# Kernel optimization log

Hardware: AMD Instinct MI355X
Metric: run time of the kernel (lower is better)

## Reference

```python
import jax, jax.numpy as jnp
import numpy as np

N = 1024; D = 128; H = 128; FF = 2048; NHEAD = 4; VOCAB = 32000; EPS = 1e-5


def _ln(x, s, b):
    m = x.mean(-1, keepdims=True)
    v = ((x - m) ** 2).mean(-1, keepdims=True)
    return (x - m) / jnp.sqrt(v + EPS) * s + b


def _mha(x, qkv_w, qkv_b, ow, ob):
    n, d = x.shape
    hd = d // NHEAD
    qkv = x @ qkv_w.T + qkv_b  # (n, 3d)
    q, k, v = [t.reshape(n, NHEAD, hd).transpose(1, 0, 2) for t in jnp.split(qkv, 3, axis=-1)]
    scores = jnp.einsum('hqd,hkd->hqk', q, k) / np.float32(np.sqrt(hd))
    attn = jax.nn.softmax(scores, axis=-1)
    o = jnp.einsum('hqk,hkd->hqd', attn, v).transpose(1, 0, 2).reshape(n, d)
    return o @ ow.T + ob


def setup_inputs() -> dict:
    key = jax.random.key(0)
    ks = jax.random.split(key, 10)
    s = 0.02
    p = lambda k, shape: (jax.random.normal(k, shape, jnp.float32) * s)
    return {
        'inputs': jax.random.randint(ks[0], (N,), 0, VOCAB),
        'emb': p(ks[1], (VOCAB, D)),
        'qkv_w': p(ks[2], (2, 3 * D, D)), 'qkv_b': jnp.zeros((2, 3 * D), jnp.float32),
        'attn_out_w': p(ks[3], (2, D, D)), 'attn_out_b': jnp.zeros((2, D), jnp.float32),
        'ln1_s': jnp.ones((2, D), jnp.float32), 'ln1_b': jnp.zeros((2, D), jnp.float32),
        'ln2_s': jnp.ones((2, D), jnp.float32), 'ln2_b': jnp.zeros((2, D), jnp.float32),
        'ff1_w': p(ks[4], (2, FF, D)), 'ff1_b': jnp.zeros((2, FF), jnp.float32),
        'ff2_w': p(ks[5], (2, D, FF)), 'ff2_b': jnp.zeros((2, D), jnp.float32),
        'w1': p(ks[6], (H, 2 * D)), 'b1': jnp.zeros((H,), jnp.float32),
        'w2': p(ks[7], (1, H)), 'b2': jnp.zeros((1,), jnp.float32),
    }


def reference(inputs, emb, qkv_w, qkv_b, attn_out_w, attn_out_b, ln1_s, ln1_b,
              ln2_s, ln2_b, ff1_w, ff1_b, ff2_w, ff2_b, w1, b1, w2, b2):
    x = emb[inputs]  # (n, d)
    for l in range(2):  # post-norm TransformerEncoderLayer (torch default)
        x = _ln(x + _mha(x, qkv_w[l], qkv_b[l], attn_out_w[l], attn_out_b[l]), ln1_s[l], ln1_b[l])
        ff = jax.nn.relu(x @ ff1_w[l].T + ff1_b[l]) @ ff2_w[l].T + ff2_b[l]
        x = _ln(x + ff, ln2_s[l], ln2_b[l])
    # pair MLP: concat(e_i, e_j) @ W1.T == e_i @ W1_left.T + e_j @ W1_right.T
    a = x @ w1[:, :D].T  # (n, H)
    b = x @ w1[:, D:].T  # (n, H)
    h = jax.nn.relu(a[:, None, :] + b[None, :, :] + b1)  # (n, n, H)
    return (h @ w2.T + b2)[..., 0]  # (n, n)
```

## Files before the change

### kernel.cpp

```cpp
#include <hip/hip_runtime.h>
#include <math.h>

#define N_TOK 1024
#define D_MODEL 128
#define NHEAD 4
#define HD 32
#define FF_DIM 2048
#define H_PAIR 128
#define QK_SCALE 0.17677669529663687f

typedef __attribute__((ext_vector_type(8))) short bf16x8;
typedef __attribute__((ext_vector_type(4))) float f32x4;

__device__ __forceinline__ unsigned short f2bf(float f) {
    unsigned u = __float_as_uint(f);
    u = u + 0x7FFFu + ((u >> 16) & 1u);
    return (unsigned short)(u >> 16);
}

__global__ void cvt4_kernel(const float* __restrict__ s0, int n0, const float* __restrict__ s1, int n1,
                            const float* __restrict__ s2, int n2, const float* __restrict__ s3, int n3,
                            unsigned short* __restrict__ d0, unsigned short* __restrict__ d1,
                            unsigned short* __restrict__ d2, unsigned short* __restrict__ d3) {
    int i = blockIdx.x * 256 + threadIdx.x;
    if (i < n0) { d0[i] = f2bf(s0[i]); return; } i -= n0;
    if (i < n1) { d1[i] = f2bf(s1[i]); return; } i -= n1;
    if (i < n2) { d2[i] = f2bf(s2[i]); return; } i -= n2;
    if (i < n3) { d3[i] = f2bf(s3[i]); }
}

__global__ void w1split_kernel(const float* __restrict__ w1, unsigned short* __restrict__ w1L,
                               unsigned short* __restrict__ w1R) {
    int h = blockIdx.x, t = threadIdx.x;
    float v = w1[h * 256 + t];
    if (t < 128) w1L[h * 128 + t] = f2bf(v);
    else         w1R[h * 128 + (t - 128)] = f2bf(v);
}

__global__ void embed_kernel(const int* __restrict__ ids, const float* __restrict__ emb,
                             float* __restrict__ x, unsigned short* __restrict__ xb) {
    int u = blockIdx.x * 256 + threadIdx.x;
    int i = u >> 5, d4 = (u & 31) * 4;
    float4 v = *(const float4*)&emb[(size_t)ids[i] * D_MODEL + d4];
    *(float4*)&x[i * D_MODEL + d4] = v;
    ushort4 bv;
    bv.x = f2bf(v.x); bv.y = f2bf(v.y); bv.z = f2bf(v.z); bv.w = f2bf(v.w);
    *(ushort4*)&xb[i * D_MODEL + d4] = bv;
}

__global__ __launch_bounds__(256) void gemm_bf(const unsigned short* __restrict__ Xb,
                                               const unsigned short* __restrict__ Wb,
                                               const unsigned short* __restrict__ Wb2,
                                               const float* __restrict__ bias,
                                               const float* __restrict__ res,
                                               float* __restrict__ Cf,
                                               unsigned short* __restrict__ Cb,
                                               float* __restrict__ part,
                                               int M, int Nc, int K, int kChunk, int act) {
    const int lane = threadIdx.x & 63;
    const int w = threadIdx.x >> 6;
    const int m0 = blockIdx.y * 64 + w * 16;
    const int n0 = blockIdx.x * 64;
    const int kb = part ? blockIdx.z * kChunk : 0;
    const int r16 = lane & 15, kh = lane >> 4;

    const unsigned short* Wsel = (Wb2 && blockIdx.z == 1) ? Wb2 : Wb;

    f32x4 acc[4] = {{0.f,0.f,0.f,0.f},{0.f,0.f,0.f,0.f},{0.f,0.f,0.f,0.f},{0.f,0.f,0.f,0.f}};
    const unsigned short* Ap = Xb + (size_t)(m0 + r16) * K + kb + kh * 8;
    const unsigned short* Bp = Wsel + (size_t)(n0 + r16) * K + kb + kh * 8;

    for (int k0 = 0; k0 < kChunk; k0 += 32) {
        bf16x8 a = *(const bf16x8*)(Ap + k0);
#pragma unroll
        for (int nt = 0; nt < 4; ++nt) {
            bf16x8 b = *(const bf16x8*)(Bp + (size_t)nt * 16 * K + k0);
            acc[nt] = __builtin_amdgcn_mfma_f32_16x16x32_bf16(a, b, acc[nt], 0, 0, 0);
        }
    }

    if (part) {
        float* P = part + (size_t)blockIdx.z * M * Nc;
#pragma unroll
        for (int nt = 0; nt < 4; ++nt) {
            int col = n0 + nt * 16 + r16;
#pragma unroll
            for (int r = 0; r < 4; ++r) {
                int row = m0 + kh * 4 + r;
                P[(size_t)row * Nc + col] = acc[nt][r];
            }
        }
    } else {
        size_t zoff = (size_t)blockIdx.z * M * Nc;
#pragma unroll
        for (int nt = 0; nt < 4; ++nt) {
            int col = n0 + nt * 16 + r16;
            float bv = bias ? bias[col] : 0.f;
#pragma unroll
            for (int r = 0; r < 4; ++r) {
                int row = m0 + kh * 4 + r;
                float v = acc[nt][r] + bv;
                if (res) v += res[(size_t)row * Nc + col];
                if (act) v = fmaxf(v, 0.f);
                if (Cf) Cf[zoff + (size_t)row * Nc + col] = v;
                if (Cb) Cb[zoff + (size_t)row * Nc + col] = f2bf(v);
            }
        }
    }
}

__global__ __launch_bounds__(256) void attn_flash(const float* __restrict__ qkv,
                                                  unsigned short* __restrict__ attn_ob) {
    const int h = blockIdx.y;
    const int q0 = blockIdx.x * 16;
    const int t = threadIdx.x;
    const int qi = t & 15;
    const int g = t >> 4;
    __shared__ float Kt[64][36];
    __shared__ float Vt[64][36];
    __shared__ float opart[16][16][36];
    __shared__ float rsum[16][17];

    float qreg[32];
    const float* Qp = qkv + (size_t)(q0 + qi) * 384 + h * HD;
#pragma unroll
    for (int d4 = 0; d4 < 8; ++d4) {
        float4 v = *(const float4*)(Qp + d4 * 4);
        qreg[d4 * 4 + 0] = v.x * QK_SCALE; qreg[d4 * 4 + 1] = v.y * QK_SCALE;
        qreg[d4 * 4 + 2] = v.z * QK_SCALE; qreg[d4 * 4 + 3] = v.w * QK_SCALE;
    }
    float opar[32] = {};
    float psum = 0.f;

    for (int j0 = 0; j0 < N_TOK; j0 += 64) {
        __syncthreads();
#pragma unroll
        for (int u = 0; u < 2; ++u) {
            int uu = t + u * 256;
            int r = uu >> 3, dq = (uu & 7) * 4;
            const float* src = qkv + (size_t)(j0 + r) * 384 + D_MODEL + h * HD + dq;
            float4 kv = *(const float4*)src;
            float4 vv = *(const float4*)(src + D_MODEL);
            *(float4*)&Kt[r][dq] = kv;
            *(float4*)&Vt[r][dq] = vv;
        }
        __syncthreads();
#pragma unroll
        for (int jj = 0; jj < 4; ++jj) {
            const int jl = g * 4 + jj;
            float s = 0.f;
#pragma unroll
            for (int d4 = 0; d4 < 8; ++d4) {
                float4 kv = *(const float4*)&Kt[jl][d4 * 4];
                s += qreg[d4 * 4 + 0] * kv.x + qreg[d4 * 4 + 1] * kv.y
                   + qreg[d4 * 4 + 2] * kv.z + qreg[d4 * 4 + 3] * kv.w;
            }
            float p = __expf(s);
            psum += p;
#pragma unroll
            for (int d4 = 0; d4 < 8; ++d4) {
                float4 vv = *(const float4*)&Vt[jl][d4 * 4];
                opar[d4 * 4 + 0] += p * vv.x; opar[d4 * 4 + 1] += p * vv.y;
                opar[d4 * 4 + 2] += p * vv.z; opar[d4 * 4 + 3] += p * vv.w;
            }
        }
    }

#pragma unroll
    for (int d4 = 0; d4 < 8; ++d4)
        *(float4*)&opart[g][qi][d4 * 4] = make_float4(opar[d4 * 4 + 0], opar[d4 * 4 + 1],
                                                      opar[d4 * 4 + 2], opar[d4 * 4 + 3]);
    rsum[qi][g] = psum;
    __syncthreads();

    {
        const int qi2 = t & 15;
        const int d0 = (t >> 4) * 2;
        float ssum = 0.f;
#pragma unroll
        for (int gg = 0; gg < 16; ++gg) ssum += rsum[qi2][gg];
        float inv = 1.0f / ssum;
        float o0 = 0.f, o1 = 0.f;
#pragma unroll
        for (int gg = 0; gg < 16; ++gg) {
            o0 += opart[gg][qi2][d0];
            o1 += opart[gg][qi2][d0 + 1];
        }
        unsigned short* dst = attn_ob + (size_t)(q0 + qi2) * D_MODEL + h * HD + d0;
        dst[0] = f2bf(o0 * inv);
        dst[1] = f2bf(o1 * inv);
    }
}

__global__ void ln_red(const float* __restrict__ in, int nz, int zstride,
                       const float* __restrict__ bias, const float* __restrict__ res,
                       const float* __restrict__ s, const float* __restrict__ b,
                       float* __restrict__ outp, unsigned short* __restrict__ outb) {
    const int i = blockIdx.x;
    const int t = threadIdx.x;
    float v0 = 0.f, v1 = 0.f;
    for (int z = 0; z < nz; ++z) {
        v0 += in[(size_t)z * zstride + i * 128 + t];
        v1 += in[(size_t)z * zstride + i * 128 + 64 + t];
    }
    if (bias) { v0 += bias[t]; v1 += bias[64 + t]; }
    if (res)  { v0 += res[i * 128 + t]; v1 += res[i * 128 + 64 + t]; }
    float sum = v0 + v1;
    for (int o = 32; o; o >>= 1) sum += __shfl_down(sum, o);
    sum = __shfl(sum, 0);
    float mean = sum * (1.0f / 128.0f);
    float d0 = v0 - mean, d1 = v1 - mean;
    float vs = d0 * d0 + d1 * d1;
    for (int o = 32; o; o >>= 1) vs += __shfl_down(vs, o);
    vs = __shfl(vs, 0);
    float inv = rsqrtf(vs * (1.0f / 128.0f) + 1e-5f);
    float r0 = d0 * inv * s[t]      + b[t];
    float r1 = d1 * inv * s[64 + t] + b[64 + t];
    outp[i * 128 + t]      = r0;
    outp[i * 128 + 64 + t] = r1;
    outb[i * 128 + t]      = f2bf(r0);
    outb[i * 128 + 64 + t] = f2bf(r1);
}

__global__ __launch_bounds__(256) void pair_kernel(const float* __restrict__ A,
                                                   const float* __restrict__ B,
                                                   const float* __restrict__ b1,
                                                   const float* __restrict__ w2,
                                                   const float* __restrict__ b2p,
                                                   float* __restrict__ outp) {
    __shared__ float As[32][132];
    __shared__ float Bs[32][132];
    __shared__ float w2s[128];
    const int t = threadIdx.x;
    const int tx = t & 15, ty = t >> 4;
    const int i0 = blockIdx.y * 32, j0 = blockIdx.x * 32;
    for (int u = t; u < 1024; u += 256) {
        int r = u >> 5, kq = (u & 31) * 4;
        float4 av = *(const float4*)&A[(size_t)(i0 + r) * 128 + kq];
        float4 bb1 = *(const float4*)&b1[kq];
        av.x += bb1.x; av.y += bb1.y; av.z += bb1.z; av.w += bb1.w;
        *(float4*)&As[r][kq] = av;
        *(float4*)&Bs[r][kq] = *(const float4*)&B[(size_t)(j0 + r) * 128 + kq];
    }
    if (t < 32) *(float4*)&w2s[t * 4] = *(const float4*)&w2[t * 4];
    __syncthreads();
    float a00 = 0.f, a01 = 0.f, a10 = 0.f, a11 = 0.f;
#pragma unroll 4
    for (int k4 = 0; k4 < 32; ++k4) {
        float4 x0 = *(const float4*)&As[ty][k4 * 4];
        float4 x1 = *(const float4*)&As[ty + 16][k4 * 4];
        float4 y0 = *(const float4*)&Bs[tx][k4 * 4];
        float4 y1 = *(const float4*)&Bs[tx + 16][k4 * 4];
        float4 w = *(const float4*)&w2s[k4 * 4];
        a00 += fmaxf(x0.x + y0.x, 0.f) * w.x + fmaxf(x0.y + y0.y, 0.f) * w.y
             + fmaxf(x0.z + y0.z, 0.f) * w.z + fmaxf(x0.w + y0.w, 0.f) * w.w;
        a01 += fmaxf(x0.x + y1.x, 0.f) * w.x + fmaxf(x0.y + y1.y, 0.f) * w.y
             + fmaxf(x0.z + y1.z, 0.f) * w.z + fmaxf(x0.w + y1.w, 0.f) * w.w;
        a10 += fmaxf(x1.x + y0.x, 0.f) * w.x + fmaxf(x1.y + y0.y, 0.f) * w.y
             + fmaxf(x1.z + y0.z, 0.f) * w.z + fmaxf(x1.w + y0.w, 0.f) * w.w;
        a11 += fmaxf(x1.x + y1.x, 0.f) * w.x + fmaxf(x1.y + y1.y, 0.f) * w.y
             + fmaxf(x1.z + y1.z, 0.f) * w.z + fmaxf(x1.w + y1.w, 0.f) * w.w;
    }
    float bb = b2p[0];
    outp[(size_t)(i0 + ty) * N_TOK + j0 + tx]            = a00 + bb;
    outp[(size_t)(i0 + ty) * N_TOK + j0 + tx + 16]       = a01 + bb;
    outp[(size_t)(i0 + ty + 16) * N_TOK + j0 + tx]       = a10 + bb;
    outp[(size_t)(i0 + ty + 16) * N_TOK + j0 + tx + 16]  = a11 + bb;
}

extern "C" void kernel_launch(void* const* d_in, const int* in_sizes, int n_in,
                              void* d_out, int out_size, void* d_ws, size_t ws_size,
                              hipStream_t stream) {
    const int*   ids   = (const int*)d_in[0];
    const float* emb   = (const float*)d_in[1];
    const float* qkv_w = (const float*)d_in[2];
    const float* qkv_b = (const float*)d_in[3];
    const float* ow    = (const float*)d_in[4];
    const float* ob    = (const float*)d_in[5];
    const float* ln1_s = (const float*)d_in[6];
    const float* ln1_b = (const float*)d_in[7];
    const float* ln2_s = (const float*)d_in[8];
    const float* ln2_b = (const float*)d_in[9];
    const float* ff1_w = (const float*)d_in[10];
    const float* ff1_b = (const float*)d_in[11];
    const float* ff2_w = (const float*)d_in[12];
    const float* ff2_b = (const float*)d_in[13];
    const float* w1    = (const float*)d_in[14];
    const float* b1    = (const float*)d_in[15];
    const float* w2    = (const float*)d_in[16];
    const float* b2    = (const float*)d_in[17];
    float* out = (float*)d_out;

    float* ws = (float*)d_ws;
    float* x        = ws;
    unsigned short* xb      = (unsigned short*)(ws + 131072);
    float* qkvb     = ws + 196608;
    unsigned short* attn_ob = (unsigned short*)(ws + 589824);
    float* tmp      = ws + 655360;
    unsigned short* ffb     = (unsigned short*)(ws + 786432);
    float* part     = ws + 1835008;
    float* pab      = ws + 2883584;
    unsigned short* qkv_wb  = (unsigned short*)(ws + 3145728);
    unsigned short* owb     = (unsigned short*)(ws + 3194880);
    unsigned short* ff1b    = (unsigned short*)(ws + 3211264);
    unsigned short* ff2b    = (unsigned short*)(ws + 3473408);
    unsigned short* w1L     = (unsigned short*)(ws + 3735552);
    unsigned short* w1R     = (unsigned short*)(ws + 3743744);

    cvt4_kernel<<<4608, 256, 0, stream>>>(qkv_w, 98304, ow, 32768, ff1_w, 524288,
                                          ff2_w, 524288, qkv_wb, owb, ff1b, ff2b);
    w1split_kernel<<<128, 256, 0, stream>>>(w1, w1L, w1R);

    embed_kernel<<<128, 256, 0, stream>>>(ids, emb, x, xb);

    for (int l = 0; l < 2; ++l) {
        const unsigned short* qwb = qkv_wb + l * 384 * 128;
        const float* qb  = qkv_b + l * 384;
        const unsigned short* owl = owb + l * 128 * 128;
        const float* obl = ob + l * 128;
        const unsigned short* f1w = ff1b + l * 2048 * 128;
        const float* f1b = ff1_b + l * 2048;
        const unsigned short* f2w = ff2b + l * 128 * 2048;
        const float* f2b = ff2_b + l * 128;

        gemm_bf<<<dim3(6, 16, 1), 256, 0, stream>>>(xb, qwb, nullptr, qb, nullptr,
                                                    qkvb, nullptr, nullptr, 1024, 384, 128, 128, 0);
        attn_flash<<<dim3(64, NHEAD), 256, 0, stream>>>(qkvb, attn_ob);
        gemm_bf<<<dim3(2, 16, 1), 256, 0, stream>>>(attn_ob, owl, nullptr, obl, x,
                                                    tmp, nullptr, nullptr, 1024, 128, 128, 128, 0);
        ln_red<<<1024, 64, 0, stream>>>(tmp, 1, 0, nullptr, nullptr,
                                        ln1_s + l * 128, ln1_b + l * 128, x, xb);
        gemm_bf<<<dim3(32, 16, 1), 256, 0, stream>>>(xb, f1w, nullptr, f1b, nullptr,
                                                     nullptr, ffb, nullptr, 1024, 2048, 128, 128, 1);
        gemm_bf<<<dim3(2, 16, 8), 256, 0, stream>>>(ffb, f2w, nullptr, nullptr, nullptr,
                                                    nullptr, nullptr, part, 1024, 128, 2048, 256, 0);
        ln_red<<<1024, 64, 0, stream>>>(part, 8, 1024 * 128, f2b, x,
                                        ln2_s + l * 128, ln2_b + l * 128, x, xb);
    }

    gemm_bf<<<dim3(2, 16, 2), 256, 0, stream>>>(xb, w1L, w1R, nullptr, nullptr,
                                                pab, nullptr, nullptr, 1024, 128, 128, 128, 0);
    pair_kernel<<<dim3(32, 32), 256, 0, stream>>>(pab, pab + 1024 * 128, b1, w2, b2, out);
}
```

Measured before the change: 283.6 us.

## Fuse out-proj, LN1, FFN, LN2 and pair projection into one per-row-block kernel

Replaces the out-projection GEMM, two LayerNorm kernels, FF1 GEMM, split-K FF2 GEMM and the final pair projection GEMM with a single kernel where each 16-row block keeps its intermediates (including the 16x2048 bf16 FF activation) in swizzled LDS. The three setup kernels are also merged into one launch. The aim is to remove several launches and the global-memory round trips for the FF activation and the split-K partials. The trade-off is that only 64 blocks run the fused stage, so parallelism is low and each block re-reads the full FF weights from global memory.

```diff
diff --git a/kernel.cpp b/kernel.cpp
--- a/kernel.cpp
+++ b/kernel.cpp
@@ -1,12 +1,6 @@
 #include <hip/hip_runtime.h>
 #include <math.h>
 
-#define N_TOK 1024
-#define D_MODEL 128
-#define NHEAD 4
-#define HD 32
-#define FF_DIM 2048
-#define H_PAIR 128
 #define QK_SCALE 0.17677669529663687f
 
 typedef __attribute__((ext_vector_type(8))) short bf16x8;
@@ -18,93 +12,66 @@
     return (unsigned short)(u >> 16);
 }
 
-__global__ void cvt4_kernel(const float* __restrict__ s0, int n0, const float* __restrict__ s1, int n1,
-                            const float* __restrict__ s2, int n2, const float* __restrict__ s3, int n3,
-                            unsigned short* __restrict__ d0, unsigned short* __restrict__ d1,
-                            unsigned short* __restrict__ d2, unsigned short* __restrict__ d3) {
-    int i = blockIdx.x * 256 + threadIdx.x;
-    if (i < n0) { d0[i] = f2bf(s0[i]); return; } i -= n0;
-    if (i < n1) { d1[i] = f2bf(s1[i]); return; } i -= n1;
-    if (i < n2) { d2[i] = f2bf(s2[i]); return; } i -= n2;
-    if (i < n3) { d3[i] = f2bf(s3[i]); }
-}
-
-__global__ void w1split_kernel(const float* __restrict__ w1, unsigned short* __restrict__ w1L,
-                               unsigned short* __restrict__ w1R) {
-    int h = blockIdx.x, t = threadIdx.x;
-    float v = w1[h * 256 + t];
-    if (t < 128) w1L[h * 128 + t] = f2bf(v);
-    else         w1R[h * 128 + (t - 128)] = f2bf(v);
-}
-
-__global__ void embed_kernel(const int* __restrict__ ids, const float* __restrict__ emb,
-                             float* __restrict__ x, unsigned short* __restrict__ xb) {
-    int u = blockIdx.x * 256 + threadIdx.x;
-    int i = u >> 5, d4 = (u & 31) * 4;
-    float4 v = *(const float4*)&emb[(size_t)ids[i] * D_MODEL + d4];
-    *(float4*)&x[i * D_MODEL + d4] = v;
-    ushort4 bv;
-    bv.x = f2bf(v.x); bv.y = f2bf(v.y); bv.z = f2bf(v.z); bv.w = f2bf(v.w);
-    *(ushort4*)&xb[i * D_MODEL + d4] = bv;
-}
-
-__global__ __launch_bounds__(256) void gemm_bf(const unsigned short* __restrict__ Xb,
-                                               const unsigned short* __restrict__ Wb,
-                                               const unsigned short* __restrict__ Wb2,
-                                               const float* __restrict__ bias,
-                                               const float* __restrict__ res,
-                                               float* __restrict__ Cf,
-                                               unsigned short* __restrict__ Cb,
-                                               float* __restrict__ part,
-                                               int M, int Nc, int K, int kChunk, int act) {
-    const int lane = threadIdx.x & 63;
-    const int w = threadIdx.x >> 6;
+__global__ void pre_kernel(const int* __restrict__ ids, const float* __restrict__ emb,
+                           const float* __restrict__ qkv_w, const float* __restrict__ ow,
+                           const float* __restrict__ ff1_w, const float* __restrict__ ff2_w,
+                           const float* __restrict__ w1,
+                           unsigned short* __restrict__ qkv_wb, unsigned short* __restrict__ owb,
+                           unsigned short* __restrict__ ff1b, unsigned short* __restrict__ ff2b,
+                           unsigned short* __restrict__ w1L, unsigned short* __restrict__ w1R,
+                           float* __restrict__ x, unsigned short* __restrict__ xb) {
+    const int blk = blockIdx.x, t = threadIdx.x;
+    if (blk < 4608) {
+        int i = blk * 256 + t;
+        if (i < 98304)       qkv_wb[i] = f2bf(qkv_w[i]);
+        else if (i < 131072) owb[i - 98304] = f2bf(ow[i - 98304]);
+        else if (i < 655360) ff1b[i - 131072] = f2bf(ff1_w[i - 131072]);
+        else                 ff2b[i - 655360] = f2bf(ff2_w[i - 655360]);
+    } else if (blk < 4736) {
+        int i = (blk - 4608) * 256 + t;
+        int h = i >> 8, c = i & 255;
+        float v = w1[i];
+        if (c < 128) w1L[h * 128 + c] = f2bf(v);
+        else         w1R[h * 128 + (c - 128)] = f2bf(v);
+    } else {
+        int u = (blk - 4736) * 256 + t;
+        int i = u >> 5, d4 = (u & 31) * 4;
+        float4 v = *(const float4*)&emb[(size_t)ids[i] * 128 + d4];
+        *(float4*)&x[i * 128 + d4] = v;
+        ushort4 bv;
+        bv.x = f2bf(v.x); bv.y = f2bf(v.y); bv.z = f2bf(v.z); bv.w = f2bf(v.w);
+        *(ushort4*)&xb[i * 128 + d4] = bv;
+    }
+}
+
+__global__ __launch_bounds__(256) void qkv_gemm(const unsigned short* __restrict__ Xb,
+                                                const unsigned short* __restrict__ Wb,
+                                                const float* __restrict__ bias,
+                                                float* __restrict__ C) {
+    const int lane = threadIdx.x & 63, w = threadIdx.x >> 6;
     const int m0 = blockIdx.y * 64 + w * 16;
     const int n0 = blockIdx.x * 64;
-    const int kb = part ? blockIdx.z * kChunk : 0;
     const int r16 = lane & 15, kh = lane >> 4;
-
-    const unsigned short* Wsel = (Wb2 && blockIdx.z == 1) ? Wb2 : Wb;
-
     f32x4 acc[4] = {{0.f,0.f,0.f,0.f},{0.f,0.f,0.f,0.f},{0.f,0.f,0.f,0.f},{0.f,0.f,0.f,0.f}};
-    const unsigned short* Ap = Xb + (size_t)(m0 + r16) * K + kb + kh * 8;
-    const unsigned short* Bp = Wsel + (size_t)(n0 + r16) * K + kb + kh * 8;
-
-    for (int k0 = 0; k0 < kChunk; k0 += 32) {
+    const unsigned short* Ap = Xb + (size_t)(m0 + r16) * 128 + kh * 8;
+    const unsigned short* Bp = Wb + (size_t)(n0 + r16) * 128 + kh * 8;
+#pragma unroll
+    for (int k0 = 0; k0 < 128; k0 += 32) {
         bf16x8 a = *(const bf16x8*)(Ap + k0);
 #pragma unroll
         for (int nt = 0; nt < 4; ++nt) {
-            bf16x8 b = *(const bf16x8*)(Bp + (size_t)nt * 16 * K + k0);
+            bf16x8 b = *(const bf16x8*)(Bp + (size_t)nt * 16 * 128 + k0);
             acc[nt] = __builtin_amdgcn_mfma_f32_16x16x32_bf16(a, b, acc[nt], 0, 0, 0);
         }
     }
-
-    if (part) {
-        float* P = part + (size_t)blockIdx.z * M * Nc;
-#pragma unroll
-        for (int nt = 0; nt < 4; ++nt) {
-            int col = n0 + nt * 16 + r16;
-#pragma unroll
-            for (int r = 0; r < 4; ++r) {
-                int row = m0 + kh * 4 + r;
-                P[(size_t)row * Nc + col] = acc[nt][r];
-            }
-        }
-    } else {
-        size_t zoff = (size_t)blockIdx.z * M * Nc;
-#pragma unroll
-        for (int nt = 0; nt < 4; ++nt) {
-            int col = n0 + nt * 16 + r16;
-            float bv = bias ? bias[col] : 0.f;
-#pragma unroll
-            for (int r = 0; r < 4; ++r) {
-                int row = m0 + kh * 4 + r;
-                float v = acc[nt][r] + bv;
-                if (res) v += res[(size_t)row * Nc + col];
-                if (act) v = fmaxf(v, 0.f);
-                if (Cf) Cf[zoff + (size_t)row * Nc + col] = v;
-                if (Cb) Cb[zoff + (size_t)row * Nc + col] = f2bf(v);
-            }
+#pragma unroll
+    for (int nt = 0; nt < 4; ++nt) {
+        int col = n0 + nt * 16 + r16;
+        float bv = bias[col];
+#pragma unroll
+        for (int r = 0; r < 4; ++r) {
+            int row = m0 + kh * 4 + r;
+            C[(size_t)row * 384 + col] = acc[nt][r] + bv;
         }
     }
 }
@@ -122,7 +89,7 @@
     __shared__ float rsum[16][17];
 
     float qreg[32];
-    const float* Qp = qkv + (size_t)(q0 + qi) * 384 + h * HD;
+    const float* Qp = qkv + (size_t)(q0 + qi) * 384 + h * 32;
 #pragma unroll
     for (int d4 = 0; d4 < 8; ++d4) {
         float4 v = *(const float4*)(Qp + d4 * 4);
@@ -132,15 +99,15 @@
     float opar[32] = {};
     float psum = 0.f;
 
-    for (int j0 = 0; j0 < N_TOK; j0 += 64) {
+    for (int j0 = 0; j0 < 1024; j0 += 64) {
         __syncthreads();
 #pragma unroll
         for (int u = 0; u < 2; ++u) {
             int uu = t + u * 256;
             int r = uu >> 3, dq = (uu & 7) * 4;
-            const float* src = qkv + (size_t)(j0 + r) * 384 + D_MODEL + h * HD + dq;
+            const float* src = qkv + (size_t)(j0 + r) * 384 + 128 + h * 32 + dq;
             float4 kv = *(const float4*)src;
-            float4 vv = *(const float4*)(src + D_MODEL);
+            float4 vv = *(const float4*)(src + 128);
             *(float4*)&Kt[r][dq] = kv;
             *(float4*)&Vt[r][dq] = vv;
         }
@@ -172,7 +139,6 @@
                                                       opar[d4 * 4 + 2], opar[d4 * 4 + 3]);
     rsum[qi][g] = psum;
     __syncthreads();
-
     {
         const int qi2 = t & 15;
         const int d0 = (t >> 4) * 2;
@@ -186,40 +152,207 @@
             o0 += opart[gg][qi2][d0];
             o1 += opart[gg][qi2][d0 + 1];
         }
-        unsigned short* dst = attn_ob + (size_t)(q0 + qi2) * D_MODEL + h * HD + d0;
+        unsigned short* dst = attn_ob + (size_t)(q0 + qi2) * 128 + h * 32 + d0;
         dst[0] = f2bf(o0 * inv);
         dst[1] = f2bf(o1 * inv);
     }
 }
 
-__global__ void ln_red(const float* __restrict__ in, int nz, int zstride,
-                       const float* __restrict__ bias, const float* __restrict__ res,
-                       const float* __restrict__ s, const float* __restrict__ b,
-                       float* __restrict__ outp, unsigned short* __restrict__ outb) {
-    const int i = blockIdx.x;
-    const int t = threadIdx.x;
-    float v0 = 0.f, v1 = 0.f;
-    for (int z = 0; z < nz; ++z) {
-        v0 += in[(size_t)z * zstride + i * 128 + t];
-        v1 += in[(size_t)z * zstride + i * 128 + 64 + t];
-    }
-    if (bias) { v0 += bias[t]; v1 += bias[64 + t]; }
-    if (res)  { v0 += res[i * 128 + t]; v1 += res[i * 128 + 64 + t]; }
-    float sum = v0 + v1;
-    for (int o = 32; o; o >>= 1) sum += __shfl_down(sum, o);
-    sum = __shfl(sum, 0);
-    float mean = sum * (1.0f / 128.0f);
-    float d0 = v0 - mean, d1 = v1 - mean;
-    float vs = d0 * d0 + d1 * d1;
-    for (int o = 32; o; o >>= 1) vs += __shfl_down(vs, o);
-    vs = __shfl(vs, 0);
-    float inv = rsqrtf(vs * (1.0f / 128.0f) + 1e-5f);
-    float r0 = d0 * inv * s[t]      + b[t];
-    float r1 = d1 * inv * s[64 + t] + b[64 + t];
-    outp[i * 128 + t]      = r0;
-    outp[i * 128 + 64 + t] = r1;
-    outb[i * 128 + t]      = f2bf(r0);
-    outb[i * 128 + 64 + t] = f2bf(r1);
+__global__ __launch_bounds__(256) void mega_mlp(
+    const unsigned short* __restrict__ attn_ob, const unsigned short* __restrict__ owb,
+    const float* __restrict__ ob, const float* __restrict__ x_res,
+    const float* __restrict__ ln1_s, const float* __restrict__ ln1_b,
+    const unsigned short* __restrict__ f1w, const float* __restrict__ f1bias,
+    const unsigned short* __restrict__ f2w, const float* __restrict__ f2bias,
+    const float* __restrict__ ln2_s, const float* __restrict__ ln2_b,
+    float* __restrict__ x_out, unsigned short* __restrict__ xb_out,
+    const unsigned short* __restrict__ w1L, const unsigned short* __restrict__ w1R,
+    float* __restrict__ pab, int do_pair) {
+    __shared__ unsigned short fflds[16 * 2048];
+    __shared__ float ylds[16][132];
+    __shared__ unsigned short xlds[16 * 128];
+    const int t = threadIdx.x, lane = t & 63, w = t >> 6;
+    const int r16 = lane & 15, kh = lane >> 4;
+    const int r0 = blockIdx.x * 16;
+
+    {
+        const int n0 = w * 32;
+        f32x4 acc[2] = {{0.f,0.f,0.f,0.f},{0.f,0.f,0.f,0.f}};
+        const unsigned short* Ap = attn_ob + (size_t)(r0 + r16) * 128 + kh * 8;
+        const unsigned short* Bp = owb + (size_t)(n0 + r16) * 128 + kh * 8;
+#pragma unroll
+        for (int k0 = 0; k0 < 128; k0 += 32) {
+            bf16x8 a = *(const bf16x8*)(Ap + k0);
+#pragma unroll
+            for (int nt = 0; nt < 2; ++nt) {
+                bf16x8 b = *(const bf16x8*)(Bp + (size_t)nt * 16 * 128 + k0);
+                acc[nt] = __builtin_amdgcn_mfma_f32_16x16x32_bf16(a, b, acc[nt], 0, 0, 0);
+            }
+        }
+#pragma unroll
+        for (int nt = 0; nt < 2; ++nt) {
+            int col = n0 + nt * 16 + r16;
+            float bv = ob[col];
+#pragma unroll
+            for (int r = 0; r < 4; ++r) {
+                int rl = kh * 4 + r;
+                ylds[rl][col] = acc[nt][r] + bv + x_res[(size_t)(r0 + rl) * 128 + col];
+            }
+        }
+    }
+    __syncthreads();
+
+    {
+        int row = t >> 4, c0 = (t & 15) * 8;
+        float4 va = *(float4*)&ylds[row][c0];
+        float4 vb = *(float4*)&ylds[row][c0 + 4];
+        float s1 = va.x + va.y + va.z + va.w + vb.x + vb.y + vb.z + vb.w;
+        float s2 = va.x*va.x + va.y*va.y + va.z*va.z + va.w*va.w
+                 + vb.x*vb.x + vb.y*vb.y + vb.z*vb.z + vb.w*vb.w;
+#pragma unroll
+        for (int o = 1; o < 16; o <<= 1) { s1 += __shfl_xor(s1, o); s2 += __shfl_xor(s2, o); }
+        float mean = s1 * (1.0f / 128.0f);
+        float inv = rsqrtf(s2 * (1.0f / 128.0f) - mean * mean + 1e-5f);
+        int sw = (row & 7) << 3;
+        unsigned short hb[8];
+        float rv[8] = {va.x, va.y, va.z, va.w, vb.x, vb.y, vb.z, vb.w};
+#pragma unroll
+        for (int j = 0; j < 8; ++j) {
+            int c = c0 + j;
+            float r = (rv[j] - mean) * inv * ln1_s[c] + ln1_b[c];
+            ylds[row][c] = r;
+            hb[j] = f2bf(r);
+        }
+        *(ushort4*)&xlds[row * 128 + (c0 ^ sw)] = make_ushort4(hb[0], hb[1], hb[2], hb[3]);
+        *(ushort4*)&xlds[row * 128 + ((c0 + 4) ^ sw)] = make_ushort4(hb[4], hb[5], hb[6], hb[7]);
+    }
+    __syncthreads();
+
+    {
+        bf16x8 a[4];
+        int swa = (r16 & 7) << 3;
+#pragma unroll
+        for (int i = 0; i < 4; ++i)
+            a[i] = *(const bf16x8*)&xlds[r16 * 128 + ((i * 32 + kh * 8) ^ swa)];
+#pragma unroll
+        for (int chunk = 0; chunk < 2; ++chunk) {
+            int cbase = w * 512 + chunk * 256;
+            f32x4 acc[16];
+#pragma unroll
+            for (int nt = 0; nt < 16; ++nt) acc[nt] = (f32x4){0.f, 0.f, 0.f, 0.f};
+#pragma unroll
+            for (int nt = 0; nt < 16; ++nt) {
+                const unsigned short* Bp = f1w + (size_t)(cbase + nt * 16 + r16) * 128 + kh * 8;
+#pragma unroll
+                for (int k0 = 0; k0 < 4; ++k0) {
+                    bf16x8 b = *(const bf16x8*)(Bp + k0 * 32);
+                    acc[nt] = __builtin_amdgcn_mfma_f32_16x16x32_bf16(a[k0], b, acc[nt], 0, 0, 0);
+                }
+            }
+#pragma unroll
+            for (int nt = 0; nt < 16; ++nt) {
+                int col = cbase + nt * 16 + r16;
+                float bv = f1bias[col];
+#pragma unroll
+                for (int r = 0; r < 4; ++r) {
+                    int row = kh * 4 + r;
+                    float v = fmaxf(acc[nt][r] + bv, 0.f);
+                    fflds[row * 2048 + (col ^ ((row & 7) << 3))] = f2bf(v);
+                }
+            }
+        }
+    }
+    __syncthreads();
+
+    {
+        const int n0 = w * 32;
+        f32x4 acc[2] = {{0.f,0.f,0.f,0.f},{0.f,0.f,0.f,0.f}};
+        int swa = (r16 & 7) << 3;
+#pragma unroll 8
+        for (int ks = 0; ks < 64; ++ks) {
+            int kk = ks * 32 + kh * 8;
+            bf16x8 a = *(const bf16x8*)&fflds[r16 * 2048 + (kk ^ swa)];
+#pragma unroll
+            for (int nt = 0; nt < 2; ++nt) {
+                bf16x8 b = *(const bf16x8*)(f2w + (size_t)(n0 + nt * 16 + r16) * 2048 + kk);
+                acc[nt] = __builtin_amdgcn_mfma_f32_16x16x32_bf16(a, b, acc[nt], 0, 0, 0);
+            }
+        }
+#pragma unroll
+        for (int nt = 0; nt < 2; ++nt) {
+            int col = n0 + nt * 16 + r16;
+            float bv = f2bias[col];
+#pragma unroll
+            for (int r = 0; r < 4; ++r) {
+                int rl = kh * 4 + r;
+                ylds[rl][col] = acc[nt][r] + bv + ylds[rl][col];
+            }
+        }
+    }
+    __syncthreads();
+
+    {
+        int row = t >> 4, c0 = (t & 15) * 8;
+        float4 va = *(float4*)&ylds[row][c0];
+        float4 vb = *(float4*)&ylds[row][c0 + 4];
+        float s1 = va.x + va.y + va.z + va.w + vb.x + vb.y + vb.z + vb.w;
+        float s2 = va.x*va.x + va.y*va.y + va.z*va.z + va.w*va.w
+                 + vb.x*vb.x + vb.y*vb.y + vb.z*vb.z + vb.w*vb.w;
+#pragma unroll
+        for (int o = 1; o < 16; o <<= 1) { s1 += __shfl_xor(s1, o); s2 += __shfl_xor(s2, o); }
+        float mean = s1 * (1.0f / 128.0f);
+        float inv = rsqrtf(s2 * (1.0f / 128.0f) - mean * mean + 1e-5f);
+        int sw = (row & 7) << 3;
+        float rv[8] = {va.x, va.y, va.z, va.w, vb.x, vb.y, vb.z, vb.w};
+        float ro[8];
+        unsigned short hb[8];
+#pragma unroll
+        for (int j = 0; j < 8; ++j) {
+            int c = c0 + j;
+            ro[j] = (rv[j] - mean) * inv * ln2_s[c] + ln2_b[c];
+            hb[j] = f2bf(ro[j]);
+        }
+        size_t gbase = (size_t)(r0 + row) * 128 + c0;
+        *(float4*)&x_out[gbase]     = make_float4(ro[0], ro[1], ro[2], ro[3]);
+        *(float4*)&x_out[gbase + 4] = make_float4(ro[4], ro[5], ro[6], ro[7]);
+        *(ushort4*)&xb_out[gbase]     = make_ushort4(hb[0], hb[1], hb[2], hb[3]);
+        *(ushort4*)&xb_out[gbase + 4] = make_ushort4(hb[4], hb[5], hb[6], hb[7]);
+        *(ushort4*)&xlds[row * 128 + (c0 ^ sw)]       = make_ushort4(hb[0], hb[1], hb[2], hb[3]);
+        *(ushort4*)&xlds[row * 128 + ((c0 + 4) ^ sw)] = make_ushort4(hb[4], hb[5], hb[6], hb[7]);
+    }
+    if (!do_pair) return;
+    __syncthreads();
+
+    {
+        bf16x8 a[4];
+        int swa = (r16 & 7) << 3;
+#pragma unroll
+        for (int i = 0; i < 4; ++i)
+            a[i] = *(const bf16x8*)&xlds[r16 * 128 + ((i * 32 + kh * 8) ^ swa)];
+        const int n0 = w * 32;
+        f32x4 accA[2] = {{0.f,0.f,0.f,0.f},{0.f,0.f,0.f,0.f}};
+        f32x4 accB[2] = {{0.f,0.f,0.f,0.f},{0.f,0.f,0.f,0.f}};
+#pragma unroll
+        for (int k0 = 0; k0 < 4; ++k0) {
+#pragma unroll
+            for (int nt = 0; nt < 2; ++nt) {
+                const unsigned short* BA = w1L + (size_t)(n0 + nt * 16 + r16) * 128 + kh * 8 + k0 * 32;
+                const unsigned short* BB = w1R + (size_t)(n0 + nt * 16 + r16) * 128 + kh * 8 + k0 * 32;
+                accA[nt] = __builtin_amdgcn_mfma_f32_16x16x32_bf16(a[k0], *(const bf16x8*)BA, accA[nt], 0, 0, 0);
+                accB[nt] = __builtin_amdgcn_mfma_f32_16x16x32_bf16(a[k0], *(const bf16x8*)BB, accB[nt], 0, 0, 0);
+            }
+        }
+#pragma unroll
+        for (int nt = 0; nt < 2; ++nt) {
+            int col = n0 + nt * 16 + r16;
+#pragma unroll
+            for (int r = 0; r < 4; ++r) {
+                int row = r0 + kh * 4 + r;
+                pab[(size_t)row * 128 + col] = accA[nt][r];
+                pab[131072 + (size_t)row * 128 + col] = accB[nt][r];
+            }
+        }
+    }
 }
 
 __global__ __launch_bounds__(256) void pair_kernel(const float* __restrict__ A,
@@ -262,10 +395,10 @@
              + fmaxf(x1.z + y1.z, 0.f) * w.z + fmaxf(x1.w + y1.w, 0.f) * w.w;
     }
     float bb = b2p[0];
-    outp[(size_t)(i0 + ty) * N_TOK + j0 + tx]            = a00 + bb;
-    outp[(size_t)(i0 + ty) * N_TOK + j0 + tx + 16]       = a01 + bb;
-    outp[(size_t)(i0 + ty + 16) * N_TOK + j0 + tx]       = a10 + bb;
-    outp[(size_t)(i0 + ty + 16) * N_TOK + j0 + tx + 16]  = a11 + bb;
+    outp[(size_t)(i0 + ty) * 1024 + j0 + tx]            = a00 + bb;
+    outp[(size_t)(i0 + ty) * 1024 + j0 + tx + 16]       = a01 + bb;
+    outp[(size_t)(i0 + ty + 16) * 1024 + j0 + tx]       = a10 + bb;
+    outp[(size_t)(i0 + ty + 16) * 1024 + j0 + tx + 16]  = a11 + bb;
 }
 
 extern "C" void kernel_launch(void* const* d_in, const int* in_sizes, int n_in,
@@ -292,53 +425,32 @@
     float* out = (float*)d_out;
 
     float* ws = (float*)d_ws;
-    float* x        = ws;
+    float*          x       = ws;
     unsigned short* xb      = (unsigned short*)(ws + 131072);
-    float* qkvb     = ws + 196608;
+    float*          qkvb    = ws + 196608;
     unsigned short* attn_ob = (unsigned short*)(ws + 589824);
-    float* tmp      = ws + 655360;
-    unsigned short* ffb     = (unsigned short*)(ws + 786432);
-    float* part     = ws + 1835008;
-    float* pab      = ws + 2883584;
-    unsigned short* qkv_wb  = (unsigned short*)(ws + 3145728);
-    unsigned short* owb     = (unsigned short*)(ws + 3194880);
-    unsigned short* ff1b    = (unsigned short*)(ws + 3211264);
-    unsigned short* ff2b    = (unsigned short*)(ws + 3473408);
-    unsigned short* w1L     = (unsigned short*)(ws + 3735552);
-    unsigned short* w1R     = (unsigned short*)(ws + 3743744);
-
-    cvt4_kernel<<<4608, 256, 0, stream>>>(qkv_w, 98304, ow, 32768, ff1_w, 524288,
-                                          ff2_w, 524288, qkv_wb, owb, ff1b, ff2b);
-    w1split_kernel<<<128, 256, 0, stream>>>(w1, w1L, w1R);
-
-    embed_kernel<<<128, 256, 0, stream>>>(ids, emb, x, xb);
+    float*          pab     = ws + 655360;
+    unsigned short* qkv_wb  = (unsigned short*)(ws + 917504);
+    unsigned short* owb     = (unsigned short*)(ws + 966656);
+    unsigned short* ff1b    = (unsigned short*)(ws + 983040);
+    unsigned short* ff2b    = (unsigned short*)(ws + 1245184);
+    unsigned short* w1L     = (unsigned short*)(ws + 1507328);
+    unsigned short* w1R     = (unsigned short*)(ws + 1515520);
+
+    pre_kernel<<<4864, 256, 0, stream>>>(ids, emb, qkv_w, ow, ff1_w, ff2_w, w1,
+                                         qkv_wb, owb, ff1b, ff2b, w1L, w1R, x, xb);
 
     for (int l = 0; l < 2; ++l) {
-        const unsigned short* qwb = qkv_wb + l * 384 * 128;
-        const float* qb  = qkv_b + l * 384;
-        const unsigned short* owl = owb + l * 128 * 128;
-        const float* obl = ob + l * 128;
-        const unsigned short* f1w = ff1b + l * 2048 * 128;
-        const float* f1b = ff1_b + l * 2048;
-        const unsigned short* f2w = ff2b + l * 128 * 2048;
-        const float* f2b = ff2_b + l * 128;
-
-        gemm_bf<<<dim3(6, 16, 1), 256, 0, stream>>>(xb, qwb, nullptr, qb, nullptr,
-                                                    qkvb, nullptr, nullptr, 1024, 384, 128, 128, 0);
-        attn_flash<<<dim3(64, NHEAD), 256, 0, stream>>>(qkvb, attn_ob);
-        gemm_bf<<<dim3(2, 16, 1), 256, 0, stream>>>(attn_ob, owl, nullptr, obl, x,
-                                                    tmp, nullptr, nullptr, 1024, 128, 128, 128, 0);
-        ln_red<<<1024, 64, 0, stream>>>(tmp, 1, 0, nullptr, nullptr,
-                                        ln1_s + l * 128, ln1_b + l * 128, x, xb);
-        gemm_bf<<<dim3(32, 16, 1), 256, 0, stream>>>(xb, f1w, nullptr, f1b, nullptr,
-                                                     nullptr, ffb, nullptr, 1024, 2048, 128, 128, 1);
-        gemm_bf<<<dim3(2, 16, 8), 256, 0, stream>>>(ffb, f2w, nullptr, nullptr, nullptr,
-                                                    nullptr, nullptr, part, 1024, 128, 2048, 256, 0);
-        ln_red<<<1024, 64, 0, stream>>>(part, 8, 1024 * 128, f2b, x,
-                                        ln2_s + l * 128, ln2_b + l * 128, x, xb);
-    }
-
-    gemm_bf<<<dim3(2, 16, 2), 256, 0, stream>>>(xb, w1L, w1R, nullptr, nullptr,
-                                                pab, nullptr, nullptr, 1024, 128, 128, 128, 0);
-    pair_kernel<<<dim3(32, 32), 256, 0, stream>>>(pab, pab + 1024 * 128, b1, w2, b2, out);
-}
+        qkv_gemm<<<dim3(6, 16), 256, 0, stream>>>(xb, qkv_wb + l * 384 * 128,
+                                                  qkv_b + l * 384, qkvb);
+        attn_flash<<<dim3(64, 4), 256, 0, stream>>>(qkvb, attn_ob);
+        mega_mlp<<<64, 256, 0, stream>>>(attn_ob, owb + l * 128 * 128, ob + l * 128, x,
+                                         ln1_s + l * 128, ln1_b + l * 128,
+                                         ff1b + l * 2048 * 128, ff1_b + l * 2048,
+                                         ff2b + l * 128 * 2048, ff2_b + l * 128,
+                                         ln2_s + l * 128, ln2_b + l * 128,
+                                         x, xb, w1L, w1R, pab, l == 1);
+    }
+
+    pair_kernel<<<dim3(32, 32), 256, 0, stream>>>(pab, pab + 131072, b1, w2, b2, out);
+}
```

Result: faster. 276.3 us (-2.6%).
